# Optimization experiments

Hardware: AMD Instinct MI355X
Metric: run time of the kernel (lower is better)

Reference implementation:

```python
import jax, jax.numpy as jnp
import numpy as np

VOCAB, EMB, HID, MAXLEN, BATCH = 32000, 256, 512, 64, 64


def setup_inputs() -> dict:
    key = jax.random.key(0)
    ks = jax.random.split(key, 12)
    s_e = 1.0 / np.sqrt(EMB)
    s_h = 1.0 / np.sqrt(HID)
    return {
        "encoder_h": jax.random.normal(ks[0], (1, BATCH, HID), jnp.float32),
        "encoder_c": jax.random.normal(ks[1], (1, BATCH, HID), jnp.float32),
        "target": jax.random.randint(ks[2], (BATCH, MAXLEN), 0, VOCAB, jnp.int64),
        "tf_mask": jax.random.randint(ks[3], (MAXLEN,), 0, 2, jnp.int32),
        "embedding": jax.random.normal(ks[4], (VOCAB, EMB), jnp.float32),
        "w_ih": jax.random.normal(ks[5], (4 * HID, EMB), jnp.float32) * s_e,
        "w_hh": jax.random.normal(ks[6], (4 * HID, HID), jnp.float32) * s_h,
        "b_ih": jax.random.normal(ks[7], (4 * HID,), jnp.float32) * s_h,
        "b_hh": jax.random.normal(ks[8], (4 * HID,), jnp.float32) * s_h,
        "fc_w": jax.random.normal(ks[9], (VOCAB, HID), jnp.float32) * s_h,
        "fc_b": jax.random.normal(ks[10], (VOCAB,), jnp.float32) * s_h,
        "target_length": 64,
    }


def reference(encoder_h, encoder_c, target, tf_mask, embedding, w_ih, w_hh,
              b_ih, b_hh, fc_w, fc_b, target_length):
    # encoder_h/c: [num_layers=1, B, H]; target: [B, T]; tf_mask: [T] (1 -> teacher forcing)
    B = target.shape[0]
    h0, c0 = encoder_h[0], encoder_c[0]              # [B, H]
    inp0 = jnp.zeros((B,), jnp.int32)                # SOS token id 0
    bias = b_ih + b_hh

    def step(carry, xs):
        h, c, inp = carry
        tgt_t, tf_t = xs
        x = embedding[inp]                           # [B, E] lookup
        gates = x @ w_ih.T + h @ w_hh.T + bias       # [B, 4H], PyTorch gate order i,f,g,o
        i, f, g, o = jnp.split(gates, 4, axis=-1)
        i, f, o = jax.nn.sigmoid(i), jax.nn.sigmoid(f), jax.nn.sigmoid(o)
        c = f * c + i * jnp.tanh(g)
        h = o * jnp.tanh(c)
        logits = h @ fc_w.T + fc_b                   # [B, V]
        greedy = jnp.argmax(logits, axis=-1).astype(jnp.int32)  # top-1 decode
        nxt = jnp.where(tf_t > 0, tgt_t, greedy)     # teacher forcing vs. greedy
        return (h, c, nxt), logits

    tgt_seq = target.T.astype(jnp.int32)             # [T, B]
    (h, c, _), outs = jax.lax.scan(step, (h0, c0, inp0), (tgt_seq, tf_mask))
    decoder_outputs = jnp.transpose(outs, (1, 0, 2))  # [B, T, V]
    return decoder_outputs, h[None], c[None]
```

## Files before the change

kernel.cpp:

```cpp
#include <hip/hip_runtime.h>
#include <cstdint>

#define VOCAB  32000
#define EMB    256
#define HID    512
#define TLEN   64
#define BATCH  64
#define G4     2048
#define OUT_LOGITS ((size_t)BATCH * TLEN * VOCAB)
#define BTV    ((size_t)TLEN * VOCAB)

typedef short s16x8 __attribute__((ext_vector_type(8)));
typedef float f32x4 __attribute__((ext_vector_type(4)));

#define WS_FCW_HI  0ull
#define WS_FCW_LO  32768000ull
#define WS_WIH_HI  65536000ull
#define WS_WIH_LO  66584576ull
#define WS_WHH_HI  67633152ull
#define WS_WHH_LO  69730304ull
#define WS_BIAS    71827456ull
#define WS_CBUF    71835648ull
#define WS_HBUF    71966720ull
#define WS_HHI     72097792ull
#define WS_HLO     72228864ull
#define WS_AMAX    72359936ull
#define WS_NEEDED  72392704ull

__device__ __forceinline__ unsigned bf16_hi_bits(float x) {
    unsigned u = __float_as_uint(x);
    return (u + 0x7FFFu + ((u >> 16) & 1u)) >> 16;
}
__device__ __forceinline__ float bf16_bits_to_f(unsigned b) {
    return __uint_as_float(b << 16);
}
__device__ __forceinline__ unsigned fkey(float x) {
    unsigned u = __float_as_uint(x);
    return (u & 0x80000000u) ? ~u : (u | 0x80000000u);
}

__global__ __launch_bounds__(256) void k_pre(
    const float* __restrict__ fcw, const float* __restrict__ wih, const float* __restrict__ whh,
    const float* __restrict__ bih, const float* __restrict__ bhh,
    const float* __restrict__ ench, const float* __restrict__ encc,
    unsigned short* fcw_hi, unsigned short* fcw_lo,
    unsigned short* wih_hi, unsigned short* wih_lo,
    unsigned short* whh_hi, unsigned short* whh_lo,
    float* bias, float* c_buf, unsigned short* hhi, unsigned short* hlo,
    unsigned long long* amax)
{
    size_t g = (size_t)blockIdx.x * 256 + threadIdx.x;
    size_t s = (size_t)gridDim.x * 256;
    for (size_t i = g; i < (size_t)VOCAB * HID; i += s) {
        float x = fcw[i]; unsigned hb = bf16_hi_bits(x);
        fcw_hi[i] = (unsigned short)hb;
        fcw_lo[i] = (unsigned short)bf16_hi_bits(x - bf16_bits_to_f(hb));
    }
    for (size_t i = g; i < (size_t)G4 * EMB; i += s) {
        float x = wih[i]; unsigned hb = bf16_hi_bits(x);
        wih_hi[i] = (unsigned short)hb;
        wih_lo[i] = (unsigned short)bf16_hi_bits(x - bf16_bits_to_f(hb));
    }
    for (size_t i = g; i < (size_t)G4 * HID; i += s) {
        float x = whh[i]; unsigned hb = bf16_hi_bits(x);
        whh_hi[i] = (unsigned short)hb;
        whh_lo[i] = (unsigned short)bf16_hi_bits(x - bf16_bits_to_f(hb));
    }
    for (size_t i = g; i < G4; i += s) bias[i] = bih[i] + bhh[i];
    for (size_t i = g; i < (size_t)BATCH * HID; i += s) {
        c_buf[i] = encc[i];
        float x = ench[i]; unsigned hb = bf16_hi_bits(x);
        hhi[(size_t)BATCH * HID + i] = (unsigned short)hb;
        hlo[(size_t)BATCH * HID + i] = (unsigned short)bf16_hi_bits(x - bf16_bits_to_f(hb));
    }
    for (size_t i = g; i < (size_t)TLEN * BATCH; i += s) amax[i] = 0ull;
}

__global__ __launch_bounds__(256) void k_cell(
    const float* __restrict__ emb,
    const unsigned short* __restrict__ wih_hi, const unsigned short* __restrict__ wih_lo,
    const unsigned short* __restrict__ whh_hi, const unsigned short* __restrict__ whh_lo,
    const float* __restrict__ bias,
    const int* __restrict__ target, const int* __restrict__ tf_mask,
    const unsigned long long* __restrict__ amax,
    float* c_buf, float* h_buf, unsigned short* hhi, unsigned short* hlo, int t)
{
    __shared__ __align__(16) unsigned short xs_hi[16 * 264];
    __shared__ __align__(16) unsigned short xs_lo[16 * 264];
    __shared__ float gbuf[4 * 16 * 16];
    __shared__ int tok_s[16];

    const int tid = threadIdx.x;
    const int jt = blockIdx.x >> 2;
    const int b0 = (blockIdx.x & 3) * 16;

    if (tid < 16) {
        int b = b0 + tid;
        int tok = 0;
        if (t > 0) {
            if (tf_mask[t - 1] > 0) tok = target[b * TLEN + (t - 1)];
            else {
                unsigned long long k = amax[(size_t)(t - 1) * BATCH + b];
                tok = (int)(~(unsigned)k);
            }
        }
        tok_s[tid] = tok;
    }
    __syncthreads();

    for (int i = tid; i < 16 * 32; i += 256) {
        int row = i >> 5, seg = i & 31;
        const float* src = emb + (size_t)tok_s[row] * EMB + seg * 8;
        int dst = row * 264 + seg * 8;
        #pragma unroll
        for (int e = 0; e < 8; e++) {
            float x = src[e]; unsigned hb = bf16_hi_bits(x);
            xs_hi[dst + e] = (unsigned short)hb;
            xs_lo[dst + e] = (unsigned short)bf16_hi_bits(x - bf16_bits_to_f(hb));
        }
    }
    __syncthreads();

    const int w = tid >> 6, l = tid & 63, li = l & 15, q = l >> 4;
    const int row0 = w * HID + jt * 16;
    const int par_r = (t + 1) & 1;
    const unsigned short* hh = hhi + (size_t)par_r * BATCH * HID;
    const unsigned short* hl = hlo + (size_t)par_r * BATCH * HID;

    f32x4 acc = {0.f, 0.f, 0.f, 0.f};
    #pragma unroll
    for (int kc = 0; kc < 8; kc++) {
        int ka = kc * 32 + q * 8;
        s16x8 ah = *(const s16x8*)(wih_hi + (size_t)(row0 + li) * EMB + ka);
        s16x8 al = *(const s16x8*)(wih_lo + (size_t)(row0 + li) * EMB + ka);
        s16x8 bh = *(const s16x8*)(xs_hi + li * 264 + ka);
        s16x8 bl = *(const s16x8*)(xs_lo + li * 264 + ka);
        acc = __builtin_amdgcn_mfma_f32_16x16x32_bf16(ah, bh, acc, 0, 0, 0);
        acc = __builtin_amdgcn_mfma_f32_16x16x32_bf16(ah, bl, acc, 0, 0, 0);
        acc = __builtin_amdgcn_mfma_f32_16x16x32_bf16(al, bh, acc, 0, 0, 0);
    }
    #pragma unroll
    for (int kc = 0; kc < 16; kc++) {
        int ka = kc * 32 + q * 8;
        s16x8 ah = *(const s16x8*)(whh_hi + (size_t)(row0 + li) * HID + ka);
        s16x8 al = *(const s16x8*)(whh_lo + (size_t)(row0 + li) * HID + ka);
        s16x8 bh = *(const s16x8*)(hh + (size_t)(b0 + li) * HID + ka);
        s16x8 bl = *(const s16x8*)(hl + (size_t)(b0 + li) * HID + ka);
        acc = __builtin_amdgcn_mfma_f32_16x16x32_bf16(ah, bh, acc, 0, 0, 0);
        acc = __builtin_amdgcn_mfma_f32_16x16x32_bf16(ah, bl, acc, 0, 0, 0);
        acc = __builtin_amdgcn_mfma_f32_16x16x32_bf16(al, bh, acc, 0, 0, 0);
    }
    #pragma unroll
    for (int r = 0; r < 4; r++) {
        int m = q * 4 + r;
        gbuf[w * 256 + m * 16 + li] = acc[r] + bias[row0 + m];
    }
    __syncthreads();

    {
        int jl = tid >> 4, bl = tid & 15;
        float gi = gbuf[0 * 256 + jl * 16 + bl];
        float gf = gbuf[1 * 256 + jl * 16 + bl];
        float gg = gbuf[2 * 256 + jl * 16 + bl];
        float go = gbuf[3 * 256 + jl * 16 + bl];
        int j = jt * 16 + jl, b = b0 + bl;
        size_t off = (size_t)b * HID + j;
        float ii = 1.f / (1.f + expf(-gi));
        float ff = 1.f / (1.f + expf(-gf));
        float oo = 1.f / (1.f + expf(-go));
        float c_new = ff * c_buf[off] + ii * tanhf(gg);
        float h_new = oo * tanhf(c_new);
        c_buf[off] = c_new;
        h_buf[off] = h_new;
        unsigned hb = bf16_hi_bits(h_new);
        size_t woff = (size_t)(t & 1) * BATCH * HID + off;
        hhi[woff] = (unsigned short)hb;
        hlo[woff] = (unsigned short)bf16_hi_bits(h_new - bf16_bits_to_f(hb));
    }
}

__global__ __launch_bounds__(256) void k_logits(
    const unsigned short* __restrict__ fcw_hi, const unsigned short* __restrict__ fcw_lo,
    const unsigned short* __restrict__ hhi, const unsigned short* __restrict__ hlo,
    const float* __restrict__ fcb, float* __restrict__ out,
    unsigned long long* __restrict__ amax_t, int t)
{
    __shared__ __align__(16) char smem[34816];
    unsigned short* sBh = (unsigned short*)smem;
    unsigned short* sBl = (unsigned short*)(smem + 17408);
    float* sOut = (float*)smem;

    const int tid = threadIdx.x;
    const int v0 = blockIdx.x * 64;
    const int w = tid >> 6, l = tid & 63, li = l & 15, q = l >> 4;
    const int par = t & 1;
    const unsigned short* hh = hhi + (size_t)par * BATCH * HID;
    const unsigned short* hl = hlo + (size_t)par * BATCH * HID;

    f32x4 acc[4] = {{0,0,0,0},{0,0,0,0},{0,0,0,0},{0,0,0,0}};

    for (int kit = 0; kit < 4; kit++) {
        int kbase = kit * 128;
        __syncthreads();
        for (int i = tid; i < 1024; i += 256) {
            int row = i >> 4, seg = i & 15;
            *(s16x8*)(sBh + row * 136 + seg * 8) = *(const s16x8*)(hh + (size_t)row * HID + kbase + seg * 8);
            *(s16x8*)(sBl + row * 136 + seg * 8) = *(const s16x8*)(hl + (size_t)row * HID + kbase + seg * 8);
        }
        __syncthreads();
        #pragma unroll
        for (int kc = 0; kc < 4; kc++) {
            int ka = kbase + kc * 32 + q * 8;
            int kl = kc * 32 + q * 8;
            s16x8 ah = *(const s16x8*)(fcw_hi + (size_t)(v0 + w * 16 + li) * HID + ka);
            s16x8 al = *(const s16x8*)(fcw_lo + (size_t)(v0 + w * 16 + li) * HID + ka);
            #pragma unroll
            for (int bt = 0; bt < 4; bt++) {
                s16x8 bh = *(const s16x8*)(sBh + (bt * 16 + li) * 136 + kl);
                s16x8 bl = *(const s16x8*)(sBl + (bt * 16 + li) * 136 + kl);
                acc[bt] = __builtin_amdgcn_mfma_f32_16x16x32_bf16(ah, bh, acc[bt], 0, 0, 0);
                acc[bt] = __builtin_amdgcn_mfma_f32_16x16x32_bf16(ah, bl, acc[bt], 0, 0, 0);
                acc[bt] = __builtin_amdgcn_mfma_f32_16x16x32_bf16(al, bh, acc[bt], 0, 0, 0);
            }
        }
    }
    __syncthreads();

    #pragma unroll
    for (int bt = 0; bt < 4; bt++) {
        #pragma unroll
        for (int r = 0; r < 4; r++) {
            int vl = w * 16 + q * 4 + r;
            int b = bt * 16 + li;
            sOut[b * 68 + vl] = acc[bt][r] + fcb[v0 + vl];
        }
    }
    __syncthreads();

    #pragma unroll
    for (int j = 0; j < 4; j++) {
        int f4 = j * 256 + tid;
        int b = f4 >> 4, v4 = f4 & 15;
        float4 val = *(const float4*)&sOut[b * 68 + v4 * 4];
        *(float4*)(out + (size_t)b * BTV + (size_t)t * VOCAB + v0 + v4 * 4) = val;
    }

    {
        int b = tid >> 2, i4 = tid & 3;
        float best = -1e38f; int bidx = 0;
        #pragma unroll
        for (int e = 0; e < 16; e++) {
            int vl = i4 * 16 + e;
            float x = sOut[b * 68 + vl];
            if (x > best) { best = x; bidx = vl; }
        }
        unsigned long long pk = ((unsigned long long)fkey(best) << 32) | (unsigned)(~(unsigned)(v0 + bidx));
        unsigned long long o1 = __shfl_xor(pk, 1); if (o1 > pk) pk = o1;
        unsigned long long o2 = __shfl_xor(pk, 2); if (o2 > pk) pk = o2;
        if (i4 == 0) atomicMax(amax_t + b, pk);
    }
}

__global__ __launch_bounds__(256) void k_tail(const float* __restrict__ h_buf,
                                              const float* __restrict__ c_buf,
                                              float* __restrict__ out)
{
    int i = blockIdx.x * 256 + threadIdx.x;
    if (i < BATCH * HID) out[OUT_LOGITS + i] = h_buf[i];
    else                 out[OUT_LOGITS + i] = c_buf[i - BATCH * HID];
}

extern "C" void kernel_launch(void* const* d_in, const int* in_sizes, int n_in,
                              void* d_out, int out_size, void* d_ws, size_t ws_size,
                              hipStream_t stream) {
    const float* ench   = (const float*)d_in[0];
    const float* encc   = (const float*)d_in[1];
    const int*   target = (const int*)d_in[2];
    const int*   tfmask = (const int*)d_in[3];
    const float* emb    = (const float*)d_in[4];
    const float* wih    = (const float*)d_in[5];
    const float* whh    = (const float*)d_in[6];
    const float* bih    = (const float*)d_in[7];
    const float* bhh    = (const float*)d_in[8];
    const float* fcw    = (const float*)d_in[9];
    const float* fcb    = (const float*)d_in[10];

    if (ws_size < WS_NEEDED) return;

    char* ws = (char*)d_ws;
    unsigned short* fcw_hi = (unsigned short*)(ws + WS_FCW_HI);
    unsigned short* fcw_lo = (unsigned short*)(ws + WS_FCW_LO);
    unsigned short* wih_hi = (unsigned short*)(ws + WS_WIH_HI);
    unsigned short* wih_lo = (unsigned short*)(ws + WS_WIH_LO);
    unsigned short* whh_hi = (unsigned short*)(ws + WS_WHH_HI);
    unsigned short* whh_lo = (unsigned short*)(ws + WS_WHH_LO);
    float* bias  = (float*)(ws + WS_BIAS);
    float* c_buf = (float*)(ws + WS_CBUF);
    float* h_buf = (float*)(ws + WS_HBUF);
    unsigned short* hhi = (unsigned short*)(ws + WS_HHI);
    unsigned short* hlo = (unsigned short*)(ws + WS_HLO);
    unsigned long long* amax = (unsigned long long*)(ws + WS_AMAX);
    float* out = (float*)d_out;

    k_pre<<<4096, 256, 0, stream>>>(fcw, wih, whh, bih, bhh, ench, encc,
                                    fcw_hi, fcw_lo, wih_hi, wih_lo, whh_hi, whh_lo,
                                    bias, c_buf, hhi, hlo, amax);

    for (int t = 0; t < TLEN; t++) {
        k_cell<<<128, 256, 0, stream>>>(emb, wih_hi, wih_lo, whh_hi, whh_lo, bias,
                                        target, tfmask, amax, c_buf, h_buf, hhi, hlo, t);
        k_logits<<<500, 256, 0, stream>>>(fcw_hi, fcw_lo, hhi, hlo, fcb, out,
                                          amax + (size_t)t * BATCH, t);
    }
    k_tail<<<256, 256, 0, stream>>>(h_buf, c_buf, out);
}
```

Measured before the change: 3.077 ms.

## Store all hidden states, batch logits into one GEMM, argmax only when greedy

Every step's hidden state is now kept in a per-timestep history buffer. All logits are produced after the recurrence by one large GEMM over 4096 rows with 256x256 tiles and swizzled LDS. The per-step vocab projection now only computes the argmax. It exits early when teacher forcing makes the greedy token unused, and it is skipped on the last step. This removes most of the per-step logits writes and reuses fc weights across many rows, at the cost of a larger workspace and high register pressure from 32 accumulators per wave.

After: 2.914 ms. -5.3%, faster.

```diff
diff --git a/kernel.cpp b/kernel.cpp
--- a/kernel.cpp
+++ b/kernel.cpp
@@ -23,9 +23,9 @@
 #define WS_CBUF    71835648ull
 #define WS_HBUF    71966720ull
 #define WS_HHI     72097792ull
-#define WS_HLO     72228864ull
-#define WS_AMAX    72359936ull
-#define WS_NEEDED  72392704ull
+#define WS_HLO     76357632ull
+#define WS_AMAX    80617472ull
+#define WS_NEEDED  80650240ull
 
 __device__ __forceinline__ unsigned bf16_hi_bits(float x) {
     unsigned u = __float_as_uint(x);
@@ -70,8 +70,8 @@
     for (size_t i = g; i < (size_t)BATCH * HID; i += s) {
         c_buf[i] = encc[i];
         float x = ench[i]; unsigned hb = bf16_hi_bits(x);
-        hhi[(size_t)BATCH * HID + i] = (unsigned short)hb;
-        hlo[(size_t)BATCH * HID + i] = (unsigned short)bf16_hi_bits(x - bf16_bits_to_f(hb));
+        hhi[i] = (unsigned short)hb;
+        hlo[i] = (unsigned short)bf16_hi_bits(x - bf16_bits_to_f(hb));
     }
     for (size_t i = g; i < (size_t)TLEN * BATCH; i += s) amax[i] = 0ull;
 }
@@ -123,9 +123,8 @@
 
     const int w = tid >> 6, l = tid & 63, li = l & 15, q = l >> 4;
     const int row0 = w * HID + jt * 16;
-    const int par_r = (t + 1) & 1;
-    const unsigned short* hh = hhi + (size_t)par_r * BATCH * HID;
-    const unsigned short* hl = hlo + (size_t)par_r * BATCH * HID;
+    const unsigned short* hh = hhi + (size_t)t * BATCH * HID;
+    const unsigned short* hl = hlo + (size_t)t * BATCH * HID;
 
     f32x4 acc = {0.f, 0.f, 0.f, 0.f};
     #pragma unroll
@@ -173,18 +172,20 @@
         c_buf[off] = c_new;
         h_buf[off] = h_new;
         unsigned hb = bf16_hi_bits(h_new);
-        size_t woff = (size_t)(t & 1) * BATCH * HID + off;
+        size_t woff = (size_t)(t + 1) * BATCH * HID + off;
         hhi[woff] = (unsigned short)hb;
         hlo[woff] = (unsigned short)bf16_hi_bits(h_new - bf16_bits_to_f(hb));
     }
 }
 
-__global__ __launch_bounds__(256) void k_logits(
+__global__ __launch_bounds__(256) void k_argmax(
     const unsigned short* __restrict__ fcw_hi, const unsigned short* __restrict__ fcw_lo,
     const unsigned short* __restrict__ hhi, const unsigned short* __restrict__ hlo,
-    const float* __restrict__ fcb, float* __restrict__ out,
+    const float* __restrict__ fcb, const int* __restrict__ tf_mask,
     unsigned long long* __restrict__ amax_t, int t)
 {
+    if (tf_mask[t] > 0) return;
+
     __shared__ __align__(16) char smem[34816];
     unsigned short* sBh = (unsigned short*)smem;
     unsigned short* sBl = (unsigned short*)(smem + 17408);
@@ -193,9 +194,8 @@
     const int tid = threadIdx.x;
     const int v0 = blockIdx.x * 64;
     const int w = tid >> 6, l = tid & 63, li = l & 15, q = l >> 4;
-    const int par = t & 1;
-    const unsigned short* hh = hhi + (size_t)par * BATCH * HID;
-    const unsigned short* hl = hlo + (size_t)par * BATCH * HID;
+    const unsigned short* hh = hhi + (size_t)(t + 1) * BATCH * HID;
+    const unsigned short* hl = hlo + (size_t)(t + 1) * BATCH * HID;
 
     f32x4 acc[4] = {{0,0,0,0},{0,0,0,0},{0,0,0,0},{0,0,0,0}};
 
@@ -237,14 +237,6 @@
     }
     __syncthreads();
 
-    #pragma unroll
-    for (int j = 0; j < 4; j++) {
-        int f4 = j * 256 + tid;
-        int b = f4 >> 4, v4 = f4 & 15;
-        float4 val = *(const float4*)&sOut[b * 68 + v4 * 4];
-        *(float4*)(out + (size_t)b * BTV + (size_t)t * VOCAB + v0 + v4 * 4) = val;
-    }
-
     {
         int b = tid >> 2, i4 = tid & 3;
         float best = -1e38f; int bidx = 0;
@@ -258,6 +250,99 @@
         unsigned long long o1 = __shfl_xor(pk, 1); if (o1 > pk) pk = o1;
         unsigned long long o2 = __shfl_xor(pk, 2); if (o2 > pk) pk = o2;
         if (i4 == 0) atomicMax(amax_t + b, pk);
+    }
+}
+
+__global__ __launch_bounds__(512) void k_blogits(
+    const unsigned short* __restrict__ fcw_hi, const unsigned short* __restrict__ fcw_lo,
+    const unsigned short* __restrict__ hhi, const unsigned short* __restrict__ hlo,
+    const float* __restrict__ fcb, float* __restrict__ out)
+{
+    __shared__ __align__(16) char smem[67584];
+    unsigned short* sBh = (unsigned short*)smem;
+    unsigned short* sBl = (unsigned short*)(smem + 32768);
+    float* sOut = (float*)smem;
+
+    const int tid = threadIdx.x;
+    const int mt = blockIdx.x & 15;
+    const int nt = blockIdx.x >> 4;
+    const int n0 = nt * 256;
+    const int ww = tid >> 6, l = tid & 63, li = l & 15, q = l >> 4;
+    const int wm = ww >> 2, wn = ww & 3;
+    const size_t hbase = ((size_t)mt * 256 + BATCH) * HID;
+
+    f32x4 acc[8][4];
+    #pragma unroll
+    for (int i = 0; i < 8; i++)
+        #pragma unroll
+        for (int j = 0; j < 4; j++) acc[i][j] = (f32x4){0.f, 0.f, 0.f, 0.f};
+
+    for (int kit = 0; kit < 8; kit++) {
+        int kbase = kit * 64;
+        __syncthreads();
+        #pragma unroll
+        for (int i2 = 0; i2 < 4; i2++) {
+            int idx = i2 * 512 + tid;
+            int row = idx >> 3, c8 = idx & 7;
+            size_t src = hbase + (size_t)row * HID + kbase + c8 * 8;
+            int dst = row * 64 + ((c8 ^ (row & 7)) << 3);
+            *(s16x8*)(sBh + dst) = *(const s16x8*)(hhi + src);
+            *(s16x8*)(sBl + dst) = *(const s16x8*)(hlo + src);
+        }
+        __syncthreads();
+        #pragma unroll
+        for (int kc = 0; kc < 2; kc++) {
+            int ka = kbase + kc * 32 + q * 8;
+            s16x8 ah[4], al[4];
+            #pragma unroll
+            for (int nf = 0; nf < 4; nf++) {
+                size_t arow = (size_t)(n0 + wn * 64 + nf * 16 + li) * HID + ka;
+                ah[nf] = *(const s16x8*)(fcw_hi + arow);
+                al[nf] = *(const s16x8*)(fcw_lo + arow);
+            }
+            #pragma unroll
+            for (int mf = 0; mf < 8; mf++) {
+                int row = wm * 128 + mf * 16 + li;
+                int ch = kc * 4 + q;
+                int off = row * 64 + (((ch ^ (row & 7)) & 7) << 3);
+                s16x8 bh = *(const s16x8*)(sBh + off);
+                s16x8 bl = *(const s16x8*)(sBl + off);
+                #pragma unroll
+                for (int nf = 0; nf < 4; nf++) {
+                    acc[mf][nf] = __builtin_amdgcn_mfma_f32_16x16x32_bf16(ah[nf], bh, acc[mf][nf], 0, 0, 0);
+                    acc[mf][nf] = __builtin_amdgcn_mfma_f32_16x16x32_bf16(ah[nf], bl, acc[mf][nf], 0, 0, 0);
+                    acc[mf][nf] = __builtin_amdgcn_mfma_f32_16x16x32_bf16(al[nf], bh, acc[mf][nf], 0, 0, 0);
+                }
+            }
+        }
+    }
+
+    for (int rd = 0; rd < 4; rd++) {
+        __syncthreads();
+        if (wm == (rd >> 1)) {
+            #pragma unroll
+            for (int mfi = 0; mfi < 4; mfi++) {
+                int mf = (rd & 1) * 4 + mfi;
+                int mrow = mf * 16 + li - (rd & 1) * 64;
+                #pragma unroll
+                for (int nf = 0; nf < 4; nf++) {
+                    #pragma unroll
+                    for (int r = 0; r < 4; r++) {
+                        int nl = wn * 64 + nf * 16 + q * 4 + r;
+                        sOut[mrow * 264 + nl] = acc[mf][nf][r] + fcb[n0 + nl];
+                    }
+                }
+            }
+        }
+        __syncthreads();
+        int tglob = mt * 4 + rd;
+        #pragma unroll
+        for (int it = 0; it < 8; it++) {
+            int idx = it * 512 + tid;
+            int row = idx >> 6, v4 = idx & 63;
+            float4 val = *(const float4*)&sOut[row * 264 + v4 * 4];
+            *(float4*)(out + (size_t)row * BTV + (size_t)tglob * VOCAB + n0 + v4 * 4) = val;
+        }
     }
 }
 
@@ -309,8 +394,12 @@
     for (int t = 0; t < TLEN; t++) {
         k_cell<<<128, 256, 0, stream>>>(emb, wih_hi, wih_lo, whh_hi, whh_lo, bias,
                                         target, tfmask, amax, c_buf, h_buf, hhi, hlo, t);
-        k_logits<<<500, 256, 0, stream>>>(fcw_hi, fcw_lo, hhi, hlo, fcb, out,
-                                          amax + (size_t)t * BATCH, t);
-    }
+        if (t < TLEN - 1)
+            k_argmax<<<500, 256, 0, stream>>>(fcw_hi, fcw_lo, hhi, hlo, fcb, tfmask,
+                                              amax + (size_t)t * BATCH, t);
+    }
+
+    k_blogits<<<2000, 512, 0, stream>>>(fcw_hi, fcw_lo, hhi, hlo, fcb, out);
+
     k_tail<<<256, 256, 0, stream>>>(h_buf, c_buf, out);
 }
```
